# Optimization experiments

Hardware: AMD Instinct MI355X
Metric: run time of the kernel (lower is better)

Reference implementation:

```python
import jax, jax.numpy as jnp
import numpy as np

N = 100_000
E = 1_600_000
IN, HID, HEADS, OUT = 128, 64, 4, 64
LAYER_DIMS = [(IN, HEADS, HID // HEADS), (HID, HEADS, HID // HEADS), (HID, 1, OUT)]
NEG_SLOPE = 0.2


def setup_inputs() -> dict:
    key = jax.random.key(0)
    ks = jax.random.split(key, 20)
    inp = {}
    inp["x"] = jax.random.normal(ks[0], (N, IN), dtype=jnp.float32)
    # edges with src != dst by construction (module removes self loops, then adds them)
    for i in range(3):
        src = jax.random.randint(ks[1 + 2 * i], (E,), 0, N, dtype=jnp.int32)
        off = jax.random.randint(ks[2 + 2 * i], (E,), 1, N, dtype=jnp.int32)
        dst = ((src + off) % N).astype(jnp.int32)
        inp[f"edge_index{i}"] = jnp.stack([src, dst])
    k = 7
    for i, (cin, h, c) in enumerate(LAYER_DIMS):
        ws = 1.0 / np.sqrt(cin)
        inp[f"Wl{i}"] = jax.random.normal(ks[k], (cin, h * c), dtype=jnp.float32) * ws; k += 1
        inp[f"bl{i}"] = jnp.zeros((h * c,), dtype=jnp.float32)
        inp[f"Wr{i}"] = jax.random.normal(ks[k], (cin, h * c), dtype=jnp.float32) * ws; k += 1
        inp[f"br{i}"] = jnp.zeros((h * c,), dtype=jnp.float32)
        inp[f"att{i}"] = jax.random.normal(ks[k], (h, c), dtype=jnp.float32) * (1.0 / np.sqrt(c)); k += 1
        inp[f"bias{i}"] = jnp.zeros((h * c,), dtype=jnp.float32)
    return inp


def _l1norm(x):
    return x / jnp.maximum(jnp.sum(jnp.abs(x), axis=1, keepdims=True), 1e-12)


def _gat2conv(x, ei, Wl, bl, Wr, br, att, bias, heads, out_c):
    n = x.shape[0]
    xl = (x @ Wl + bl).reshape(n, heads, out_c)  # source-side features (x_j)
    xr = (x @ Wr + br).reshape(n, heads, out_c)  # target-side features (x_i)
    src, dst = ei[0], ei[1]
    s = jax.nn.leaky_relu(xl[src] + xr[dst], NEG_SLOPE)      # [E', H, C]
    a = jnp.einsum('ehc,hc->eh', s, att)                      # [E', H]
    m = jax.ops.segment_max(a, dst, num_segments=n)           # segment softmax over edges per target
    e = jnp.exp(a - m[dst])
    den = jax.ops.segment_sum(e, dst, num_segments=n)
    alpha = e / (den[dst] + 1e-16)
    msg = (xl[src] * alpha[:, :, None]).reshape(-1, heads * out_c)
    return jax.ops.segment_sum(msg, dst, num_segments=n) + bias  # concat heads + bias


def _forward(x, eis, params):
    loop = jnp.arange(N, dtype=eis[0].dtype)
    self_loops = jnp.stack([loop, loop])
    num_layers = len(LAYER_DIMS)
    for i, ((cin, h, c), p) in enumerate(zip(LAYER_DIMS, params)):
        ei = jnp.concatenate([eis[i], self_loops], axis=1)  # add_self_loops
        new_x = _gat2conv(x, ei, *p, h, c)
        x = new_x
        if i != num_layers - 1:
            x = jax.nn.relu(new_x)
        x = _l1norm(x)  # F.normalize(x, p=1)
    x = x / jnp.maximum(jnp.linalg.norm(x, axis=1, keepdims=True), 1e-12)  # F.normalize (L2)
    return jax.nn.relu(x)


def reference(x, edge_index0, edge_index1, edge_index2,
              Wl0, bl0, Wr0, br0, att0, bias0,
              Wl1, bl1, Wr1, br1, att1, bias1,
              Wl2, bl2, Wr2, br2, att2, bias2):
    eis = (edge_index0, edge_index1, edge_index2)
    params = [(Wl0, bl0, Wr0, br0, att0, bias0),
              (Wl1, bl1, Wr1, br1, att1, bias1),
              (Wl2, bl2, Wr2, br2, att2, bias2)]
    return _forward(x, eis, params)
```

## Files before the change

kernel.cpp:

```cpp
#include <hip/hip_runtime.h>
#include <hip/hip_fp16.h>
#include <string.h>

#define NN 100000
#define EE 1600000
#define CAP 64
#define NBIN 196
#define BINSZ 512
#define BINCAP 10400
#define CHA 4096
#define NCA 391
#define GGX 391

typedef __fp16 h2v __attribute__((ext_vector_type(2)));
typedef __fp16 half8 __attribute__((ext_vector_type(8)));
typedef float  f32x4 __attribute__((ext_vector_type(4)));

template<int CTRL>
__device__ __forceinline__ float dppadd(float x){
    int y = __builtin_amdgcn_update_dpp(0, __float_as_int(x), CTRL, 0xF, 0xF, true);
    return x + __int_as_float(y);
}
template<int H>
__device__ __forceinline__ float head_reduce32(float p){
    p = dppadd<0xB1>(p);
    p = dppadd<0x4E>(p);
    p = dppadd<0x141>(p);
    if constexpr (H == 1){
        p = dppadd<0x140>(p);
        p += __shfl_xor(p, 16);
    }
    return p;
}
__device__ __forceinline__ float red32(float p){
    p = dppadd<0xB1>(p);
    p = dppadd<0x4E>(p);
    p = dppadd<0x141>(p);
    p = dppadd<0x140>(p);
    p += __shfl_xor(p, 16);
    return p;
}


__global__ __launch_bounds__(256) void k_A(
    const int* __restrict__ e0, const int* __restrict__ e1, const int* __restrict__ e2,
    int2* __restrict__ p0, int2* __restrict__ p1, int2* __restrict__ p2,
    int* __restrict__ tail)
{
    __shared__ int shist[NBIN], lbase[NBIN], gbase[NBIN], cur[NBIN];
    __shared__ int sd[CHA], ss[CHA], spp[CHA];
    const int l = blockIdx.x / NCA, c = blockIdx.x % NCA;
    const int* ei = (l==0? e0 : l==1? e1 : e2);
    int2* pr = (l==0? p0 : l==1? p1 : p2);
    const int base = c*CHA, n = min(CHA, EE-base);
    const int tid = threadIdx.x;
    for (int i=tid;i<NBIN;i+=256) shist[i]=0;
    __syncthreads();
    for (int i=tid;i<n;i+=256) atomicAdd(&shist[ei[EE+base+i]>>9],1);
    __syncthreads();
    if (tid==0){ int acc=0; for (int i=0;i<NBIN;++i){ lbase[i]=acc; acc+=shist[i]; } }
    __syncthreads();
    if (tid<NBIN){ gbase[tid] = atomicAdd(&tail[l*NBIN+tid], shist[tid]); cur[tid]=lbase[tid]; }
    __syncthreads();
    for (int i=tid;i<n;i+=256){
        const int d = ei[EE+base+i], s = ei[base+i];
        const int bb = d>>9;
        const int r = atomicAdd(&cur[bb],1);
        const int off = gbase[bb] + (r - lbase[bb]);
        sd[r]=d; ss[r]=s;
        spp[r] = (off < BINCAP) ? (bb*BINCAP + off) : -1;
    }
    __syncthreads();
    for (int i=tid;i<n;i+=256){ const int p = spp[i]; if (p >= 0) pr[p] = make_int2(sd[i], ss[i]); }
}

__global__ __launch_bounds__(256) void k_B(
    const int2* __restrict__ p0, const int2* __restrict__ p1, const int2* __restrict__ p2,
    const int* __restrict__ tail,
    int* __restrict__ c0, int* __restrict__ s0,
    int* __restrict__ c1, int* __restrict__ s1,
    int* __restrict__ c2, int* __restrict__ s2)
{
    __shared__ int cnt[BINSZ];
    __shared__ __align__(16) int sl[BINSZ*CAP];
    const int l = blockIdx.x / NBIN, b = blockIdx.x % NBIN;
    const int2* pr = (l==0? p0 : l==1? p1 : p2) + (size_t)b*BINCAP;
    int* gc = (l==0? c0 : l==1? c1 : c2);
    int* gs = (l==0? s0 : l==1? s1 : s2);
    const int n0 = b*BINSZ;
    const int nn = min(BINSZ, NN - n0);
    const int tid = threadIdx.x;
    for (int i=tid;i<nn;i+=256){ cnt[i]=1; sl[i*CAP]= n0+i; }
    __syncthreads();
    const int ec = min(tail[l*NBIN+b], BINCAP);
    for (int i=tid;i<ec;i+=256){
        const int2 e = pr[i];
        const int nd = e.x - n0;
        const int p = atomicAdd(&cnt[nd],1);
        if (p < CAP) sl[nd*CAP+p] = e.y;
    }
    __syncthreads();
    for (int i=tid;i<nn;i+=256) gc[n0+i] = cnt[i];
    const int t4 = nn*(CAP/4);
    int4* gs4 = (int4*)(gs + (size_t)n0*CAP);
    const int4* sl4 = (const int4*)sl;
    for (int i=tid;i<t4;i+=256) gs4[i] = sl4[i];
}


template<int CIN>
__global__ __launch_bounds__(256) void k_gemm(
    const float* __restrict__ x,
    const float* __restrict__ Wl, const float* __restrict__ bl,
    const float* __restrict__ Wr, const float* __restrict__ br,
    __half* __restrict__ xlh, float* __restrict__ xr)
{
    constexpr int KC = CIN / 32;
    const int tid = threadIdx.x;
    const int wave = tid >> 6, lane = tid & 63;
    const int m = lane & 15, g = lane >> 4;
    const int side = blockIdx.y;
    const float* __restrict__ W  = side ? Wr : Wl;
    const float* __restrict__ bb = side ? br : bl;

    half8 bf[4][KC];
    #pragma unroll
    for (int ct = 0; ct < 4; ++ct)
        #pragma unroll
        for (int kc = 0; kc < KC; ++kc)
            #pragma unroll
            for (int i = 0; i < 8; ++i)
                bf[ct][kc][i] = (__fp16)W[(kc*32 + g*8 + i)*64 + ct*16 + m];

    float bv[4];
    #pragma unroll
    for (int ct = 0; ct < 4; ++ct) bv[ct] = bb[ct*16 + m];

    const int stride = GGX * 64;
    for (int row0 = blockIdx.x*64 + wave*16; row0 < NN; row0 += stride){
        half8 a[KC];
        const float* xp = x + (size_t)(row0 + m) * CIN + g*8;
        #pragma unroll
        for (int kc = 0; kc < KC; ++kc){
            const float4 u = *(const float4*)(xp + kc*32);
            const float4 v = *(const float4*)(xp + kc*32 + 4);
            a[kc][0]=(__fp16)u.x; a[kc][1]=(__fp16)u.y; a[kc][2]=(__fp16)u.z; a[kc][3]=(__fp16)u.w;
            a[kc][4]=(__fp16)v.x; a[kc][5]=(__fp16)v.y; a[kc][6]=(__fp16)v.z; a[kc][7]=(__fp16)v.w;
        }
        f32x4 acc0 = {0,0,0,0}, acc1 = {0,0,0,0}, acc2 = {0,0,0,0}, acc3 = {0,0,0,0};
        #pragma unroll
        for (int kc = 0; kc < KC; ++kc){
            acc0 = __builtin_amdgcn_mfma_f32_16x16x32_f16(a[kc], bf[0][kc], acc0, 0,0,0);
            acc1 = __builtin_amdgcn_mfma_f32_16x16x32_f16(a[kc], bf[1][kc], acc1, 0,0,0);
            acc2 = __builtin_amdgcn_mfma_f32_16x16x32_f16(a[kc], bf[2][kc], acc2, 0,0,0);
            acc3 = __builtin_amdgcn_mfma_f32_16x16x32_f16(a[kc], bf[3][kc], acc3, 0,0,0);
        }
        #pragma unroll
        for (int j = 0; j < 4; ++j){
            const size_t rb = (size_t)(row0 + 4*g + j)*64 + m;
            const float o0 = acc0[j] + bv[0];
            const float o1 = acc1[j] + bv[1];
            const float o2 = acc2[j] + bv[2];
            const float o3 = acc3[j] + bv[3];
            if (side){
                xr[rb]    = o0; xr[rb+16] = o1; xr[rb+32] = o2; xr[rb+48] = o3;
            } else {
                xlh[rb]    = __float2half_rn(o0);
                xlh[rb+16] = __float2half_rn(o1);
                xlh[rb+32] = __float2half_rn(o2);
                xlh[rb+48] = __float2half_rn(o3);
            }
        }
    }
}

template<int H, bool LAST>
__global__ __launch_bounds__(256) void k_fused(
    const int* __restrict__ cnt, const int* __restrict__ slots,
    const __half* __restrict__ xlh, const float* __restrict__ xr,
    const float* __restrict__ att, const float* __restrict__ bias,
    float* __restrict__ out)
{
    const int lane = threadIdx.x & 63;
    const int hl = lane >> 5;
    const int c  = lane & 31;
    const int node = __builtin_amdgcn_readfirstlane(blockIdx.x * 4 + (threadIdx.x >> 6));
    if (node >= NN) return;

    const float2 xr2f = *(const float2*)(xr + (size_t)node*64 + 2*c);
    const h2v xr2 = { (__fp16)xr2f.x, (__fp16)xr2f.y };
    const float2 at2f = *(const float2*)(att + 2*c);
    const h2v at2 = { (__fp16)(at2f.x * 1.44269504088896f),
                      (__fp16)(at2f.y * 1.44269504088896f) };
    const float2 bias2 = *(const float2*)(bias + 2*c);
    const h2v k02 = { (__fp16)0.2f, (__fp16)0.2f };

    int deg = __builtin_amdgcn_readfirstlane(cnt[node]);
    deg = deg > CAP ? CAP : deg;
    const int dm1 = deg - 1;
    const int* __restrict__ sp = slots + (size_t)node * CAP;

    float den = 0.f, a0 = 0.f, a1 = 0.f;
    const int ngrp = (deg + 7) >> 3;

    for (int g = 0; g < ngrp; ++g){
        const int b0 = g*8;
        int ein[4]; h2v x2[4]; float q[4], e[4];
        #pragma unroll
        for (int j = 0; j < 4; ++j){
            ein[j] = b0 + 2*j + hl;
            const int ec = ein[j] < dm1 ? ein[j] : dm1;
            const int id = sp[ec];
            x2[j] = *(const h2v*)(xlh + (size_t)id*64 + 2*c);
        }
        #pragma unroll
        for (int j = 0; j < 4; ++j){
            h2v v = x2[j] + xr2;
            v = __builtin_elementwise_max(v, v * k02);
            q[j] = head_reduce32<H>(__builtin_amdgcn_fdot2(v, at2, 0.f, false));
        }
        if (b0 + 8 > deg){
            #pragma unroll
            for (int j = 0; j < 4; ++j) if (ein[j] > dm1) q[j] = -16384.f;
        }
        #pragma unroll
        for (int j = 0; j < 4; ++j) e[j] = __builtin_amdgcn_exp2f(q[j]);
        #pragma unroll
        for (int j = 0; j < 4; ++j){
            a0 = fmaf(e[j], (float)x2[j][0], a0);
            a1 = fmaf(e[j], (float)x2[j][1], a1);
        }
        den += (e[0]+e[1]) + (e[2]+e[3]);
    }
    a0 += __shfl_xor(a0, 32);
    a1 += __shfl_xor(a1, 32);
    den += __shfl_xor(den, 32);

    const float rd = __builtin_amdgcn_rcpf(den);
    float o0 = fmaf(a0, rd, bias2.x);
    float o1 = fmaf(a1, rd, bias2.y);
    if (!LAST){ o0 = fmaxf(o0, 0.f); o1 = fmaxf(o1, 0.f); }
    const float ns = red32(fabsf(o0) + fabsf(o1));
    const float rs = __builtin_amdgcn_rcpf(fmaxf(ns, 1e-12f));
    o0 *= rs; o1 *= rs;
    if (LAST){
        const float qq = red32(o0*o0 + o1*o1);
        const float rq = __builtin_amdgcn_rsqf(fmaxf(qq, 1e-24f));
        o0 = fmaxf(o0*rq, 0.f); o1 = fmaxf(o1*rq, 0.f);
    }
    if (hl == 0) *(float2*)(out + (size_t)node*64 + 2*c) = make_float2(o0, o1);
}

__global__ __launch_bounds__(256) void k_init(int* __restrict__ cnt, int* __restrict__ slots)
{
    const int i = blockIdx.x * 256 + threadIdx.x;
    if (i < NN){ cnt[i] = 1; slots[(size_t)i * CAP] = i; }
}
__global__ __launch_bounds__(256) void k_build(
    const int* __restrict__ ei, int* __restrict__ cnt, int* __restrict__ slots)
{
    const int stride = gridDim.x * 256;
    for (int e = blockIdx.x * 256 + threadIdx.x; e < EE; e += stride){
        const int s = ei[e], d = ei[e + EE];
        const int pos = atomicAdd(&cnt[d], 1);
        if (pos < CAP) slots[(size_t)d * CAP + pos] = s;
    }
}

extern "C" void kernel_launch(void* const* d_in, const int* in_sizes, int n_in,
                              void* d_out, int out_size, void* d_ws, size_t ws_size,
                              hipStream_t stream)
{
    const float* x0 = (const float*)d_in[0];
    const int* ei[3] = {(const int*)d_in[1], (const int*)d_in[2], (const int*)d_in[3]};
    const float *Wl[3], *bl[3], *Wr[3], *br[3], *att[3], *bias[3];
    for (int i = 0; i < 3; ++i){
        Wl[i]   = (const float*)d_in[4 + 6*i];
        bl[i]   = (const float*)d_in[5 + 6*i];
        Wr[i]   = (const float*)d_in[6 + 6*i];
        br[i]   = (const float*)d_in[7 + 6*i];
        att[i]  = (const float*)d_in[8 + 6*i];
        bias[i] = (const float*)d_in[9 + 6*i];
    }
    float* out = (float*)d_out;

    const size_t NN64 = (size_t)NN * 64;
    __half* xlh = (__half*)d_ws;
    float*  xr  = (float*)((char*)d_ws + NN64*2);
    float*  xb  = out;
    int* base = (int*)(xr + NN64);

    const size_t fused_need = NN64*2 + NN64*4 + (3*(size_t)NN*(CAP+1) + 3*NBIN)*4;

    dim3 blk(256);
    dim3 ggrid2(GGX, 2);
    const int ngrid = (NN + 3) / 4;
    const int igrid = (NN + 255) / 256;

    if (ws_size >= fused_need){
        int* c0 = base;                 int* s0 = c0 + NN;
        int* c1 = s0 + (size_t)NN*CAP;  int* s1 = c1 + NN;
        int* c2 = s1 + (size_t)NN*CAP;  int* s2 = c2 + NN;
        int* tail = s2 + (size_t)NN*CAP;
        int2* p0 = (int2*)out;
        int2* p1 = (int2*)d_ws;
        int2* p2 = p1 + (size_t)NBIN*BINCAP;

        (void)hipMemsetAsync(tail, 0, 3*NBIN*sizeof(int), stream);
        k_A<<<3*NCA, blk, 0, stream>>>(ei[0], ei[1], ei[2], p0, p1, p2, tail);
        k_B<<<3*NBIN, blk, 0, stream>>>(p0, p1, p2, tail, c0, s0, c1, s1, c2, s2);

        k_gemm<128><<<ggrid2, blk, 0, stream>>>(x0, Wl[0], bl[0], Wr[0], br[0], xlh, xr);
        k_fused<4,false><<<ngrid, blk, 0, stream>>>(c0, s0, xlh, xr, att[0], bias[0], xb);
        k_gemm<64><<<ggrid2, blk, 0, stream>>>(xb, Wl[1], bl[1], Wr[1], br[1], xlh, xr);
        k_fused<4,false><<<ngrid, blk, 0, stream>>>(c1, s1, xlh, xr, att[1], bias[1], xb);
        k_gemm<64><<<ggrid2, blk, 0, stream>>>(xb, Wl[2], bl[2], Wr[2], br[2], xlh, xr);
        k_fused<1,true><<<ngrid, blk, 0, stream>>>(c2, s2, xlh, xr, att[2], bias[2], out);
    } else {
        int* cnt = base;
        int* slots = cnt + NN;

        k_init<<<igrid, blk, 0, stream>>>(cnt, slots);
        k_gemm<128><<<ggrid2, blk, 0, stream>>>(x0, Wl[0], bl[0], Wr[0], br[0], xlh, xr);
        k_build<<<512, blk, 0, stream>>>(ei[0], cnt, slots);
        k_fused<4,false><<<ngrid, blk, 0, stream>>>(cnt, slots, xlh, xr, att[0], bias[0], xb);

        k_init<<<igrid, blk, 0, stream>>>(cnt, slots);
        k_gemm<64><<<ggrid2, blk, 0, stream>>>(xb, Wl[1], bl[1], Wr[1], br[1], xlh, xr);
        k_build<<<512, blk, 0, stream>>>(ei[1], cnt, slots);
        k_fused<4,false><<<ngrid, blk, 0, stream>>>(cnt, slots, xlh, xr, att[1], bias[1], xb);

        k_init<<<igrid, blk, 0, stream>>>(cnt, slots);
        k_gemm<64><<<ggrid2, blk, 0, stream>>>(xb, Wl[2], bl[2], Wr[2], br[2], xlh, xr);
        k_build<<<512, blk, 0, stream>>>(ei[2], cnt, slots);
        k_fused<1,true><<<ngrid, blk, 0, stream>>>(cnt, slots, xlh, xr, att[2], bias[2], out);
    }
}
```

Before: 338.3 us.

## Pack edge pairs into one int, register-cache edges, per-wave histograms in binning

The binning kernel now packs each (src, local dst) pair into a single 32-bit int (src<<9 | dst&511), which halves the intermediate bucket buffer traffic between the two CSR build kernels. Edges are loaded once into registers instead of being re-read from global memory for the histogram and scatter passes. The histogram uses per-wave shared copies to reduce atomic contention. Chunk size is halved to 2048, doubling the block count. Packing relies on src < 2^23 and a bin size of 512, and the smaller chunks mean more global tail atomics.

```diff
diff --git a/kernel.cpp b/kernel.cpp
--- a/kernel.cpp
+++ b/kernel.cpp
@@ -8,8 +8,8 @@
 #define NBIN 196
 #define BINSZ 512
 #define BINCAP 10400
-#define CHA 4096
-#define NCA 391
+#define CHA 2048
+#define NCA 782
 #define GGX 391
 
 typedef __fp16 h2v __attribute__((ext_vector_type(2)));
@@ -44,38 +44,53 @@
 
 __global__ __launch_bounds__(256) void k_A(
     const int* __restrict__ e0, const int* __restrict__ e1, const int* __restrict__ e2,
-    int2* __restrict__ p0, int2* __restrict__ p1, int2* __restrict__ p2,
+    int* __restrict__ p0, int* __restrict__ p1, int* __restrict__ p2,
     int* __restrict__ tail)
 {
+    __shared__ int h4[4][NBIN];
     __shared__ int shist[NBIN], lbase[NBIN], gbase[NBIN], cur[NBIN];
-    __shared__ int sd[CHA], ss[CHA], spp[CHA];
+    __shared__ int pk[CHA], spp[CHA];
     const int l = blockIdx.x / NCA, c = blockIdx.x % NCA;
     const int* ei = (l==0? e0 : l==1? e1 : e2);
-    int2* pr = (l==0? p0 : l==1? p1 : p2);
+    int* pr = (l==0? p0 : l==1? p1 : p2);
     const int base = c*CHA, n = min(CHA, EE-base);
     const int tid = threadIdx.x;
-    for (int i=tid;i<NBIN;i+=256) shist[i]=0;
-    __syncthreads();
-    for (int i=tid;i<n;i+=256) atomicAdd(&shist[ei[EE+base+i]>>9],1);
+    const int wave = tid >> 6;
+    for (int i=tid;i<4*NBIN;i+=256) ((int*)h4)[i]=0;
+    __syncthreads();
+    int dreg[CHA/256], sreg[CHA/256];
+    #pragma unroll
+    for (int j = 0; j < CHA/256; ++j){
+        const int i = tid + j*256;
+        if (i < n){ dreg[j] = ei[EE+base+i]; sreg[j] = ei[base+i]; }
+        else { dreg[j] = -1; }
+    }
+    #pragma unroll
+    for (int j = 0; j < CHA/256; ++j)
+        if (dreg[j] >= 0) atomicAdd(&h4[wave][dreg[j]>>9],1);
+    __syncthreads();
+    for (int i=tid;i<NBIN;i+=256) shist[i] = h4[0][i]+h4[1][i]+h4[2][i]+h4[3][i];
     __syncthreads();
     if (tid==0){ int acc=0; for (int i=0;i<NBIN;++i){ lbase[i]=acc; acc+=shist[i]; } }
     __syncthreads();
     if (tid<NBIN){ gbase[tid] = atomicAdd(&tail[l*NBIN+tid], shist[tid]); cur[tid]=lbase[tid]; }
     __syncthreads();
-    for (int i=tid;i<n;i+=256){
-        const int d = ei[EE+base+i], s = ei[base+i];
+    #pragma unroll
+    for (int j = 0; j < CHA/256; ++j){
+        if (dreg[j] < 0) continue;
+        const int d = dreg[j], s = sreg[j];
         const int bb = d>>9;
         const int r = atomicAdd(&cur[bb],1);
         const int off = gbase[bb] + (r - lbase[bb]);
-        sd[r]=d; ss[r]=s;
+        pk[r] = (s << 9) | (d & 511);
         spp[r] = (off < BINCAP) ? (bb*BINCAP + off) : -1;
     }
     __syncthreads();
-    for (int i=tid;i<n;i+=256){ const int p = spp[i]; if (p >= 0) pr[p] = make_int2(sd[i], ss[i]); }
+    for (int i=tid;i<n;i+=256){ const int p = spp[i]; if (p >= 0) pr[p] = pk[i]; }
 }
 
 __global__ __launch_bounds__(256) void k_B(
-    const int2* __restrict__ p0, const int2* __restrict__ p1, const int2* __restrict__ p2,
+    const int* __restrict__ p0, const int* __restrict__ p1, const int* __restrict__ p2,
     const int* __restrict__ tail,
     int* __restrict__ c0, int* __restrict__ s0,
     int* __restrict__ c1, int* __restrict__ s1,
@@ -84,7 +99,7 @@
     __shared__ int cnt[BINSZ];
     __shared__ __align__(16) int sl[BINSZ*CAP];
     const int l = blockIdx.x / NBIN, b = blockIdx.x % NBIN;
-    const int2* pr = (l==0? p0 : l==1? p1 : p2) + (size_t)b*BINCAP;
+    const int* pr = (l==0? p0 : l==1? p1 : p2) + (size_t)b*BINCAP;
     int* gc = (l==0? c0 : l==1? c1 : c2);
     int* gs = (l==0? s0 : l==1? s1 : s2);
     const int n0 = b*BINSZ;
@@ -94,10 +109,10 @@
     __syncthreads();
     const int ec = min(tail[l*NBIN+b], BINCAP);
     for (int i=tid;i<ec;i+=256){
-        const int2 e = pr[i];
-        const int nd = e.x - n0;
+        const int pv = pr[i];
+        const int nd = pv & 511;
         const int p = atomicAdd(&cnt[nd],1);
-        if (p < CAP) sl[nd*CAP+p] = e.y;
+        if (p < CAP) sl[nd*CAP+p] = pv >> 9;
     }
     __syncthreads();
     for (int i=tid;i<nn;i+=256) gc[n0+i] = cnt[i];
@@ -302,9 +317,9 @@
         int* c1 = s0 + (size_t)NN*CAP;  int* s1 = c1 + NN;
         int* c2 = s1 + (size_t)NN*CAP;  int* s2 = c2 + NN;
         int* tail = s2 + (size_t)NN*CAP;
-        int2* p0 = (int2*)out;
-        int2* p1 = (int2*)d_ws;
-        int2* p2 = p1 + (size_t)NBIN*BINCAP;
+        int* p0 = (int*)out;
+        int* p1 = (int*)d_ws;
+        int* p2 = p1 + (size_t)NBIN*BINCAP;
 
         (void)hipMemsetAsync(tail, 0, 3*NBIN*sizeof(int), stream);
         k_A<<<3*NCA, blk, 0, stream>>>(ei[0], ei[1], ei[2], p0, p1, p2, tail);
```

Result: no change. 339.5 us (+0.4%).
